# Performance work log

Hardware: AMD Instinct MI355X
Metric: run time of the kernel (lower is better)

The kernel has to match this reference:

```python
import jax, jax.numpy as jnp
import numpy as np

INF_NUMBER = 1.0e12
ZERO_TOL = 1e-9
NEG_SLOPE = 0.2

B, G, N = 16, 128, 512
P, E, K, F = 4, 1, 3, 128


def setup_inputs() -> dict:
    key = jax.random.key(0)
    k1, k2, k3, k4, k5, k6, k7 = jax.random.split(key, 7)
    x = jax.random.normal(k1, (B, G, N), dtype=jnp.float32)
    u = jax.random.uniform(k2, (B, E, N, N), dtype=jnp.float32)
    S = jnp.where(u < 0.1, u, 0.0)
    std = 1.0 / np.sqrt(G * P)
    W = jax.random.uniform(k3, (P, E, G, G), minval=-std, maxval=std, dtype=jnp.float32)
    mixer = jax.random.uniform(k4, (P, E, 2 * F), minval=-std, maxval=std, dtype=jnp.float32)
    h = jax.random.uniform(k5, (P, F, E, K, G), minval=-std, maxval=std, dtype=jnp.float32)
    b = jax.random.uniform(k6, (F, 1), minval=-std, maxval=std, dtype=jnp.float32)
    return {"x": x, "S": S, "W": W, "mixer": mixer, "h": h, "b": b}


def _attention_gso(x, W, S):
    # x: (B,G,N); W: (P,E,G,G); S: (B,E,N,N)
    # Wx = W @ x_query : (B,P,E,G,N)
    Wx = jnp.einsum('pegh,bhn->bpegn', W, x)
    # xWx = x_key @ Wx : (B,P,E,N,N)  (x_key[b,m,g] = x[b,g,m])
    xWx = jnp.einsum('bgm,bpegn->bpemn', x, Wx)
    eij = jax.nn.leaky_relu(xWx, negative_slope=NEG_SLOPE)
    # edge mask from |S| summed over edge features: (B,1,1,N,N)
    mask = (jnp.sum(jnp.abs(S), axis=1) > ZERO_TOL).astype(x.dtype)[:, None, None]
    scores = eij * mask - (1.0 - mask) * INF_NUMBER
    aij = jax.nn.softmax(scores, axis=-1) * mask
    return aij  # (B,P,E,N,N)


def reference(x, S, W, mixer, h, b):
    # mixer is declared by the torch module but unused in key-query mode
    aij = _attention_gso(x, W, S)  # (B,P,E,N,N)
    # K-hop taps: z[k] = x @ aij^k, broadcast over (P,E)
    xk = jnp.broadcast_to(x[:, None, None], (B, P, E, G, N))
    taps = [xk]
    for _ in range(1, K):
        xk = jnp.einsum('bpegn,bpenm->bpegm', xk, aij)
        taps.append(xk)
    z = jnp.stack(taps, axis=3)  # (B,P,E,K,G,N)
    # filter GEMM: contract over (E,K,G) -> (B,P,F,N)
    y = jnp.einsum('bpekgn,pfekg->bpfn', z, h) + b  # b: (F,1) broadcasts
    # concatenate heads: relu then (B, P*F, N)
    y = jax.nn.relu(y)
    y = jnp.transpose(y, (0, 3, 1, 2)).reshape(B, N, P * F)
    return jnp.transpose(y, (0, 2, 1))
```

## Files before the change

### kernel.cpp

```cpp
#include <hip/hip_runtime.h>

#define Bx 16
#define Gx 128
#define Nx 512
#define Px 4
#define Kx 3
#define Fx 128
#define NEG_SLOPE 0.2f
#define ZERO_TOL 1e-9f
#define BIGF 1.0e30f

typedef unsigned short u16;
typedef unsigned int u32;
typedef __bf16 v8bf __attribute__((ext_vector_type(8)));
typedef _Float16 v8hf __attribute__((ext_vector_type(8)));
typedef float v4f __attribute__((ext_vector_type(4)));

__device__ __forceinline__ u16 f2b(float f) {
  union { float f; u32 u; } v; v.f = f;
  u32 r = (v.u + 0x7fffu + ((v.u >> 16) & 1u)) >> 16;
  return (u16)r;
}
__device__ __forceinline__ u16 f2h(float f) {
  union { _Float16 h; u16 u; } v; v.h = (_Float16)f;
  return v.u;
}

#define G2L16(gsrc, ldst)                                                     \
  __builtin_amdgcn_global_load_lds(                                           \
      (const __attribute__((address_space(1))) void*)(gsrc),                  \
      (__attribute__((address_space(3))) void*)(ldst), 16, 0, 0)

__global__ __launch_bounds__(256) void prep_kernel(const float* __restrict__ S,
                                                   const float* __restrict__ x,
                                                   const float* __restrict__ W,
                                                   const float* __restrict__ h,
                                                   u32* __restrict__ mb,
                                                   u16* __restrict__ xb,
                                                   u16* __restrict__ xTb,
                                                   u16* __restrict__ xT16,
                                                   u16* __restrict__ w16,
                                                   u16* __restrict__ Hb) {
  const int blk = blockIdx.x;
  const int tid = threadIdx.x;
  __shared__ float t[32][33];
  if (blk < 512) {
    const int wi = blk * 256 + tid;
    const float4* S4 = (const float4*)S;
    u32 bits = 0;
#pragma unroll
    for (int q = 0; q < 8; q++) {
      float4 v = S4[(size_t)wi * 8 + q];
      bits |= (fabsf(v.x) > ZERO_TOL ? 1u : 0u) << (q * 4);
      bits |= (fabsf(v.y) > ZERO_TOL ? 2u : 0u) << (q * 4);
      bits |= (fabsf(v.z) > ZERO_TOL ? 4u : 0u) << (q * 4);
      bits |= (fabsf(v.w) > ZERO_TOL ? 8u : 0u) << (q * 4);
    }
    mb[wi] = bits;
  } else if (blk < 1536) {
    const int idx = blk - 512;
    const int b = idx >> 6, g0 = ((idx >> 4) & 3) * 32, n0 = (idx & 15) * 32;
    const int r = tid >> 3, c4 = (tid & 7) * 4;
    const float* xp = x + (size_t)b * Gx * Nx;
    float4 v = *(const float4*)&xp[(g0 + r) * Nx + n0 + c4];
    ushort4 o;
    o.x = f2b(v.x); o.y = f2b(v.y); o.z = f2b(v.z); o.w = f2b(v.w);
    *(ushort4*)&xb[(size_t)b * Gx * Nx + (g0 + r) * Nx + n0 + c4] = o;
    t[r][c4 + 0] = v.x; t[r][c4 + 1] = v.y; t[r][c4 + 2] = v.z; t[r][c4 + 3] = v.w;
    __syncthreads();
    float tv[4] = {t[c4 + 0][r], t[c4 + 1][r], t[c4 + 2][r], t[c4 + 3][r]};
    ushort4 ob, oh;
    ob.x = f2b(tv[0]); oh.x = f2h(tv[0]);
    ob.y = f2b(tv[1]); oh.y = f2h(tv[1]);
    ob.z = f2b(tv[2]); oh.z = f2h(tv[2]);
    ob.w = f2b(tv[3]); oh.w = f2h(tv[3]);
    size_t off = (size_t)b * Nx * Gx + (size_t)(n0 + r) * Gx + g0 + c4;
    *(ushort4*)&xTb[off] = ob;
    *(ushort4*)&xT16[off] = oh;
  } else if (blk < 1600) {
    int i4 = ((blk - 1536) * 256 + tid) * 4;
    float4 v = *(const float4*)&W[i4];
    ushort4 o;
    o.x = f2h(v.x); o.y = f2h(v.y); o.z = f2h(v.z); o.w = f2h(v.w);
    *(ushort4*)&w16[i4] = o;
  } else {
    int i4 = ((blk - 1600) * 256 + tid) * 4;
    float4 v = *(const float4*)&h[i4];
    ushort4 o;
    o.x = f2b(v.x); o.y = f2b(v.y); o.z = f2b(v.z); o.w = f2b(v.w);
    *(ushort4*)&Hb[i4] = o;
  }
}

__global__ __launch_bounds__(256) void wxt16_kernel(const u16* __restrict__ xT16,
                                                    const u16* __restrict__ w16,
                                                    u16* __restrict__ WxT16) {
  __shared__ __align__(16) char smem[49152];
  constexpr int OB = 16384;
  const int bp = blockIdx.x, b = bp >> 2, p = bp & 3;
  const int rt = blockIdx.y;
  const int tid = threadIdx.x;
  const int w = tid >> 6, l = tid & 63;
  const int wr = w >> 1, wc = w & 1;
  const int lr = l & 15, ks = l >> 4;

  const u16* Ap = xT16 + ((size_t)b * Nx + rt * 64) * Gx;
  const u16* Bp = w16 + (size_t)p * Gx * Gx;
#pragma unroll
  for (int it = 0; it < 4; it++) {
    int chunk = it * 256 + w * 64 + l;
    int r = chunk >> 4, kq = l & 15;
    int kg = (kq ^ (r & 15)) * 8;
    G2L16(Ap + (size_t)r * Gx + kg, smem + it * 4096 + w * 1024);
  }
#pragma unroll
  for (int it = 0; it < 8; it++) {
    int chunk = it * 256 + w * 64 + l;
    int r = chunk >> 4, kq = l & 15;
    int kg = (kq ^ (r & 15)) * 8;
    G2L16(Bp + (size_t)r * Gx + kg, smem + OB + it * 4096 + w * 1024);
  }
  __syncthreads();

  v4f acc[2][4];
#pragma unroll
  for (int fr = 0; fr < 2; fr++)
#pragma unroll
    for (int fc = 0; fc < 4; fc++) acc[fr][fc] = (v4f){0.f, 0.f, 0.f, 0.f};

#pragma unroll
  for (int t = 0; t < 4; t++) {
    int kk = t * 4 + ks;
    v8hf ah[2];
#pragma unroll
    for (int fr = 0; fr < 2; fr++) {
      int ra = wr * 32 + fr * 16 + lr;
      ah[fr] = *(const v8hf*)(smem + ra * 256 + ((kk ^ (ra & 15)) * 16));
    }
#pragma unroll
    for (int fc = 0; fc < 4; fc++) {
      int rb = wc * 64 + fc * 16 + lr;
      v8hf bh = *(const v8hf*)(smem + OB + rb * 256 + ((kk ^ (rb & 15)) * 16));
#pragma unroll
      for (int fr = 0; fr < 2; fr++)
        acc[fr][fc] = __builtin_amdgcn_mfma_f32_16x16x32_f16(ah[fr], bh, acc[fr][fc], 0, 0, 0);
    }
  }

  u16* op = WxT16 + (size_t)bp * Nx * Gx;
#pragma unroll
  for (int fr = 0; fr < 2; fr++)
#pragma unroll
    for (int fc = 0; fc < 4; fc++) {
      int n = rt * 64 + wr * 32 + fr * 16 + ks * 4;
      int g = wc * 64 + fc * 16 + lr;
#pragma unroll
      for (int q = 0; q < 4; q++) op[(size_t)(n + q) * Gx + g] = f2h(acc[fr][fc][q]);
    }
}

__global__ __launch_bounds__(512, 4) void attn5_kernel(const u16* __restrict__ xT16,
                                                       const u16* __restrict__ WxT16,
                                                       const u32* __restrict__ mb,
                                                       u16* __restrict__ aijT) {
  __shared__ __align__(16) char smem[71680];
  constexpr int OMBS = 65536, ORED = 69632;
  const int bp = blockIdx.x, b = bp >> 2;
  const int i0 = blockIdx.y * 64;
  const int tid = threadIdx.x;
  const int w = tid >> 6, l = tid & 63;
  const int wr = w >> 2, wc = w & 3;
  const int lr = l & 15, ks = l >> 4;

  {
    const u32* mbp = mb + ((size_t)b * Nx + i0) * 16;
    u32* mbs = (u32*)(smem + OMBS);
    mbs[tid] = mbp[tid];
    mbs[tid + 512] = mbp[tid + 512];
  }
  {
    const u16* Ap = xT16 + ((size_t)b * Nx + i0) * Gx;
#pragma unroll
    for (int it = 0; it < 2; it++) {
      int chunk = it * 512 + w * 64 + l;
      int r = chunk >> 4, kq = l & 15;
      int kg = (kq ^ (r & 15)) * 8;
      G2L16(Ap + (size_t)r * Gx + kg, smem + it * 8192 + w * 1024);
    }
  }
  __syncthreads();

  v8hf areg[2][4];
#pragma unroll
  for (int fr = 0; fr < 2; fr++) {
    int ra = wr * 32 + fr * 16 + lr;
#pragma unroll
    for (int t = 0; t < 4; t++) {
      int kk = t * 4 + ks;
      areg[fr][t] = *(const v8hf*)(smem + ra * 256 + ((kk ^ (ra & 15)) * 16));
    }
  }
  __syncthreads();

  const u16* Bp = WxT16 + (size_t)bp * Nx * Gx;
  auto STAGE_B = [&](int t) {
    char* dst = smem + (t & 1) * 32768;
    int g0 = t * 32;
#pragma unroll
    for (int it = 0; it < 4; it++) {
      int chunk = it * 512 + w * 64 + l;
      int r = chunk >> 2, kq = l & 3;
      int kg = (kq ^ (r & 3)) * 8;
      G2L16(Bp + (size_t)r * Gx + g0 + kg, dst + it * 8192 + w * 1024);
    }
  };

  v4f acc[2][8];
#pragma unroll
  for (int fr = 0; fr < 2; fr++)
#pragma unroll
    for (int fc = 0; fc < 8; fc++) acc[fr][fc] = (v4f){0.f, 0.f, 0.f, 0.f};

  STAGE_B(0);
  for (int t = 0; t < 4; t++) {
    __syncthreads();
    if (t < 3) STAGE_B(t + 1);
    const char* bb = smem + (t & 1) * 32768;
#pragma unroll
    for (int fc = 0; fc < 8; fc++) {
      int rb = wc * 128 + fc * 16 + lr;
      v8hf bh = *(const v8hf*)(bb + rb * 64 + ((ks ^ (rb & 3)) * 16));
#pragma unroll
      for (int fr = 0; fr < 2; fr++)
        acc[fr][fc] = __builtin_amdgcn_mfma_f32_16x16x32_f16(areg[fr][t], bh, acc[fr][fc], 0, 0, 0);
    }
  }

  u32* mbs = (u32*)(smem + OMBS);
  float* red0 = (float*)(smem + ORED);
  float* red1 = red0 + 256;

#pragma unroll
  for (int fr = 0; fr < 2; fr++)
#pragma unroll
    for (int q = 0; q < 4; q++) {
      int row = wr * 32 + fr * 16 + ks * 4 + q;
      float m = -BIGF;
#pragma unroll
      for (int fc = 0; fc < 8; fc++) {
        u32 word = mbs[row * 16 + wc * 4 + (fc >> 1)];
        int bit = ((fc & 1) << 4) + lr;
        float v = acc[fr][fc][q];
        v = v >= 0.f ? v : NEG_SLOPE * v;
        v = ((word >> bit) & 1u) ? v : -BIGF;
        acc[fr][fc][q] = v;
        m = fmaxf(m, v);
      }
      m = fmaxf(m, __shfl_xor(m, 1, 64));
      m = fmaxf(m, __shfl_xor(m, 2, 64));
      m = fmaxf(m, __shfl_xor(m, 4, 64));
      m = fmaxf(m, __shfl_xor(m, 8, 64));
      if (lr == 0) red0[row * 4 + wc] = m;
    }
  __syncthreads();
#pragma unroll
  for (int fr = 0; fr < 2; fr++)
#pragma unroll
    for (int q = 0; q < 4; q++) {
      int row = wr * 32 + fr * 16 + ks * 4 + q;
      float4 pm = *(const float4*)&red0[row * 4];
      float gm = fmaxf(fmaxf(pm.x, pm.y), fmaxf(pm.z, pm.w));
      float s = 0.f;
#pragma unroll
      for (int fc = 0; fc < 8; fc++) {
        float v = acc[fr][fc][q];
        float e = (v <= -0.5f * BIGF) ? 0.f : __expf(v - gm);
        acc[fr][fc][q] = e;
        s += e;
      }
      s += __shfl_xor(s, 1, 64);
      s += __shfl_xor(s, 2, 64);
      s += __shfl_xor(s, 4, 64);
      s += __shfl_xor(s, 8, 64);
      if (lr == 0) red1[row * 4 + wc] = s;
    }
  __syncthreads();
  u16* dst = aijT + (size_t)bp * Nx * Nx + i0;
#pragma unroll
  for (int fr = 0; fr < 2; fr++) {
    int rbase = wr * 32 + fr * 16 + ks * 4;
    float inv[4];
#pragma unroll
    for (int q = 0; q < 4; q++) {
      float4 ps = *(const float4*)&red1[(rbase + q) * 4];
      float tot = (ps.x + ps.y) + (ps.z + ps.w);
      inv[q] = tot > 0.f ? 1.f / tot : 0.f;
    }
#pragma unroll
    for (int fc = 0; fc < 8; fc++) {
      int j = wc * 128 + fc * 16 + lr;
      ushort4 pk;
      pk.x = f2b(acc[fr][fc][0] * inv[0]);
      pk.y = f2b(acc[fr][fc][1] * inv[1]);
      pk.z = f2b(acc[fr][fc][2] * inv[2]);
      pk.w = f2b(acc[fr][fc][3] * inv[3]);
      *(ushort4*)&dst[(size_t)j * Nx + rbase] = pk;
    }
  }
}

template <int MODE>
__global__ __launch_bounds__(256) void gnt_kernel(const u16* __restrict__ pA,
                                                  const u16* __restrict__ pB,
                                                  const u16* __restrict__ pC,
                                                  const u16* __restrict__ pHb,
                                                  u16* __restrict__ o1,
                                                  u16* __restrict__ o2,
                                                  float* __restrict__ oF,
                                                  const float* __restrict__ bias) {
  __shared__ __align__(16) char smem[2][12288];
  const int bp = blockIdx.x;
  const int b = bp >> 2, p = bp & 3;
  const int by = blockIdx.y;
  const int rt = (MODE == 1) ? (by >> 2) : by;
  const int ct = (MODE == 1) ? (by & 3) : 0;
  const int tid = threadIdx.x;
  const int w = tid >> 6, l = tid & 63;
  const int wr = w >> 1, wc = w & 1;
  const int lr = l & 15, kslot = l >> 4;

  constexpr int KTOT = (MODE == 2) ? (Kx * Gx) : Nx;
  constexpr int SA = (MODE == 2) ? Gx : Nx;
  constexpr int SB = (MODE == 2) ? (Kx * Gx) : Nx;
  constexpr int NT = KTOT / 32;

  const u16* Abase;
  const u16* Bbase;
  if (MODE == 0) {
    Abase = pA + (size_t)bp * Nx * Nx + (size_t)rt * 64 * Nx;
    Bbase = pB + (size_t)b * Gx * Nx;
  } else if (MODE == 1) {
    Abase = pA + (size_t)bp * Gx * Nx + (size_t)rt * 64 * Nx;
    Bbase = pB + (size_t)bp * Nx * Nx + (size_t)ct * 128 * Nx;
  } else {
    Abase = nullptr;
    Bbase = pHb + (size_t)p * Fx * (Kx * Gx);
  }

  const int sar = tid >> 2;
  const int sakg = (tid & 3) ^ (sar & 3);
  const int sbr0 = tid >> 2, sbkg0 = (tid & 3) ^ (sbr0 & 3);
  const int sbr1 = (tid + 256) >> 2, sbkg1 = (tid & 3) ^ (sbr1 & 3);

  int aoff[2], boff[4];
#pragma unroll
  for (int fr = 0; fr < 2; fr++) {
    int row = wr * 32 + fr * 16 + lr;
    aoff[fr] = row * 64 + ((kslot ^ (row & 3)) * 16);
  }
#pragma unroll
  for (int fc = 0; fc < 4; fc++) {
    int row = wc * 64 + fc * 16 + lr;
    boff[fc] = 4096 + row * 64 + ((kslot ^ (row & 3)) * 16);
  }

  auto STAGE = [&](int bufi, int k0) {
    const u16* Aseg;
    int kin;
    if (MODE == 2) {
      int seg = k0 >> 7;
      kin = k0 & 127;
      const u16* base = (seg == 0) ? (pA + (size_t)b * Nx * Gx)
                       : (seg == 1) ? (pB + (size_t)bp * Nx * Gx)
                                    : (pC + (size_t)bp * Nx * Gx);
      Aseg = base + (size_t)rt * 64 * Gx;
    } else {
      Aseg = Abase;
      kin = k0;
    }
    char* base = smem[bufi];
    G2L16(Aseg + (size_t)sar * SA + kin + sakg * 8, base + w * 1024);
    G2L16(Bbase + (size_t)sbr0 * SB + k0 + sbkg0 * 8, base + 4096 + w * 1024);
    G2L16(Bbase + (size_t)sbr1 * SB + k0 + sbkg1 * 8, base + 8192 + w * 1024);
  };

  v4f acc[2][4];
#pragma unroll
  for (int fr = 0; fr < 2; fr++)
#pragma unroll
    for (int fc = 0; fc < 4; fc++) acc[fr][fc] = (v4f){0.f, 0.f, 0.f, 0.f};

  STAGE(0, 0);
  int cur = 0;
  for (int t = 0; t < NT; t++) {
    __syncthreads();
    if (t + 1 < NT) STAGE(cur ^ 1, (t + 1) * 32);
    const char* bb = smem[cur];
    v8bf af[2], bf4[4];
#pragma unroll
    for (int fr = 0; fr < 2; fr++) af[fr] = *(const v8bf*)(bb + aoff[fr]);
#pragma unroll
    for (int fc = 0; fc < 4; fc++) bf4[fc] = *(const v8bf*)(bb + boff[fc]);
#pragma unroll
    for (int fr = 0; fr < 2; fr++)
#pragma unroll
      for (int fc = 0; fc < 4; fc++)
        acc[fr][fc] = __builtin_amdgcn_mfma_f32_16x16x32_bf16(af[fr], bf4[fc],
                                                              acc[fr][fc], 0, 0, 0);
    cur ^= 1;
  }

  if (MODE == 0) {
    u16* z1p = o1 + (size_t)bp * Gx * Nx;
    u16* z1Tp = o2 + (size_t)bp * Nx * Gx;
#pragma unroll
    for (int fr = 0; fr < 2; fr++)
#pragma unroll
      for (int fc = 0; fc < 4; fc++) {
        int m0 = rt * 64 + wr * 32 + fr * 16 + kslot * 4;
        int g = wc * 64 + fc * 16 + lr;
        v4f a = acc[fr][fc];
        ushort4 pk;
        pk.x = f2b(a[0]); pk.y = f2b(a[1]); pk.z = f2b(a[2]); pk.w = f2b(a[3]);
        *(ushort4*)&z1p[(size_t)g * Nx + m0] = pk;
        z1Tp[(size_t)(m0 + 0) * Gx + g] = pk.x;
        z1Tp[(size_t)(m0 + 1) * Gx + g] = pk.y;
        z1Tp[(size_t)(m0 + 2) * Gx + g] = pk.z;
        z1Tp[(size_t)(m0 + 3) * Gx + g] = pk.w;
      }
  } else if (MODE == 1) {
    u16* z2Tp = o1 + (size_t)bp * Nx * Gx;
#pragma unroll
    for (int fr = 0; fr < 2; fr++)
#pragma unroll
      for (int fc = 0; fc < 4; fc++) {
        int g0r = rt * 64 + wr * 32 + fr * 16 + kslot * 4;
        int m = ct * 128 + wc * 64 + fc * 16 + lr;
        v4f a = acc[fr][fc];
        ushort4 pk;
        pk.x = f2b(a[0]); pk.y = f2b(a[1]); pk.z = f2b(a[2]); pk.w = f2b(a[3]);
        *(ushort4*)&z2Tp[(size_t)m * Gx + g0r] = pk;
      }
  } else {
    float* op = oF + (size_t)(b * Px + p) * Fx * Nx;
#pragma unroll
    for (int fc = 0; fc < 4; fc++) {
      int f = wc * 64 + fc * 16 + lr;
      float bi = bias[f];
#pragma unroll
      for (int fr = 0; fr < 2; fr++) {
        int n0 = rt * 64 + wr * 32 + fr * 16 + kslot * 4;
        v4f a = acc[fr][fc];
        float4 o;
        o.x = fmaxf(a[0] + bi, 0.f);
        o.y = fmaxf(a[1] + bi, 0.f);
        o.z = fmaxf(a[2] + bi, 0.f);
        o.w = fmaxf(a[3] + bi, 0.f);
        *(float4*)&op[(size_t)f * Nx + n0] = o;
      }
    }
  }
}

extern "C" void kernel_launch(void* const* d_in, const int* in_sizes, int n_in,
                              void* d_out, int out_size, void* d_ws, size_t ws_size,
                              hipStream_t stream) {
  const float* x = (const float*)d_in[0];
  const float* S = (const float*)d_in[1];
  const float* W = (const float*)d_in[2];
  const float* h = (const float*)d_in[4];
  const float* bias = (const float*)d_in[5];
  float* out = (float*)d_out;

  char* ws = (char*)d_ws;
  u16* aijT  = (u16*)ws;
  u16* WxT16 = (u16*)(ws + 33554432);
  u16* xT16  = (u16*)(ws + 41943040);
  u16* xTb   = (u16*)(ws + 44040192);
  u16* xb    = (u16*)(ws + 46137344);
  u16* z1    = (u16*)(ws + 48234496);
  u16* z1T   = (u16*)(ws + 56623104);
  u16* z2T   = (u16*)(ws + 65011712);
  u16* Hb    = (u16*)(ws + 73400320);
  u16* W16   = (u16*)(ws + 73793536);
  u32* mb    = (u32*)(ws + 73924608);

  prep_kernel<<<dim3(1792), 256, 0, stream>>>(S, x, W, h, mb, xb, xTb, xT16, W16, Hb);
  wxt16_kernel<<<dim3(Bx * Px, Nx / 64), 256, 0, stream>>>(xT16, W16, WxT16);
  attn5_kernel<<<dim3(Bx * Px, Nx / 64), 512, 0, stream>>>(xT16, WxT16, mb, aijT);
  gnt_kernel<0><<<dim3(Bx * Px, 8), 256, 0, stream>>>(aijT, xb, nullptr, nullptr,
                                                      z1, z1T, nullptr, nullptr);
  gnt_kernel<1><<<dim3(Bx * Px, 8), 256, 0, stream>>>(z1, aijT, nullptr, nullptr,
                                                      z2T, nullptr, nullptr, nullptr);
  gnt_kernel<2><<<dim3(Bx * Px, 8), 256, 0, stream>>>(xTb, z1T, z2T, Hb,
                                                      nullptr, nullptr, out, bias);
  (void)in_sizes; (void)n_in; (void)out_size; (void)ws_size;
}
```

Measured before the change: 78.82 us.

## Fuse second hop with filter GEMM and single-buffer attention staging

Fuses the second K-hop GEMM with the filter GEMM, so z2 stays in LDS as a swizzled tile instead of being written to global memory and read back. This removes one launch and the z2T round trip. The attention kernel drops double buffering of the Wx tiles to shrink LDS from about 70KB to 38KB, trading copy/compute overlap for more resident blocks. The mask-packing prep now uses wave ballots over coalesced loads instead of per-thread float4 bit packing.

```diff
diff --git a/kernel.cpp b/kernel.cpp
--- a/kernel.cpp
+++ b/kernel.cpp
@@ -12,6 +12,7 @@
 
 typedef unsigned short u16;
 typedef unsigned int u32;
+typedef unsigned long long u64;
 typedef __bf16 v8bf __attribute__((ext_vector_type(8)));
 typedef _Float16 v8hf __attribute__((ext_vector_type(8)));
 typedef float v4f __attribute__((ext_vector_type(4)));
@@ -45,18 +46,14 @@
   const int tid = threadIdx.x;
   __shared__ float t[32][33];
   if (blk < 512) {
-    const int wi = blk * 256 + tid;
-    const float4* S4 = (const float4*)S;
-    u32 bits = 0;
-#pragma unroll
-    for (int q = 0; q < 8; q++) {
-      float4 v = S4[(size_t)wi * 8 + q];
-      bits |= (fabsf(v.x) > ZERO_TOL ? 1u : 0u) << (q * 4);
-      bits |= (fabsf(v.y) > ZERO_TOL ? 2u : 0u) << (q * 4);
-      bits |= (fabsf(v.z) > ZERO_TOL ? 4u : 0u) << (q * 4);
-      bits |= (fabsf(v.w) > ZERO_TOL ? 8u : 0u) << (q * 4);
-    }
-    mb[wi] = bits;
+    const int w = tid >> 6, l = tid & 63;
+    const size_t base = (size_t)blk * 8192;
+#pragma unroll 4
+    for (int i = 0; i < 32; i++) {
+      float v = S[base + i * 256 + tid];
+      u64 m = __ballot(fabsf(v) > ZERO_TOL);
+      if (l == 0) *(u64*)&mb[(base + i * 256 + w * 64) >> 5] = m;
+    }
   } else if (blk < 1536) {
     const int idx = blk - 512;
     const int b = idx >> 6, g0 = ((idx >> 4) & 3) * 32, n0 = (idx & 15) * 32;
@@ -159,12 +156,12 @@
     }
 }
 
-__global__ __launch_bounds__(512, 4) void attn5_kernel(const u16* __restrict__ xT16,
+__global__ __launch_bounds__(512, 4) void attn7_kernel(const u16* __restrict__ xT16,
                                                        const u16* __restrict__ WxT16,
                                                        const u32* __restrict__ mb,
                                                        u16* __restrict__ aijT) {
-  __shared__ __align__(16) char smem[71680];
-  constexpr int OMBS = 65536, ORED = 69632;
+  __shared__ __align__(16) char smem[38912];
+  constexpr int OMBS = 32768, ORED = 36864;
   const int bp = blockIdx.x, b = bp >> 2;
   const int i0 = blockIdx.y * 64;
   const int tid = threadIdx.x;
@@ -202,38 +199,32 @@
   }
   __syncthreads();
 
+  v4f acc[2][8];
+#pragma unroll
+  for (int fr = 0; fr < 2; fr++)
+#pragma unroll
+    for (int fc = 0; fc < 8; fc++) acc[fr][fc] = (v4f){0.f, 0.f, 0.f, 0.f};
+
   const u16* Bp = WxT16 + (size_t)bp * Nx * Gx;
-  auto STAGE_B = [&](int t) {
-    char* dst = smem + (t & 1) * 32768;
+  for (int t = 0; t < 4; t++) {
     int g0 = t * 32;
 #pragma unroll
     for (int it = 0; it < 4; it++) {
       int chunk = it * 512 + w * 64 + l;
       int r = chunk >> 2, kq = l & 3;
       int kg = (kq ^ (r & 3)) * 8;
-      G2L16(Bp + (size_t)r * Gx + g0 + kg, dst + it * 8192 + w * 1024);
-    }
-  };
-
-  v4f acc[2][8];
-#pragma unroll
-  for (int fr = 0; fr < 2; fr++)
-#pragma unroll
-    for (int fc = 0; fc < 8; fc++) acc[fr][fc] = (v4f){0.f, 0.f, 0.f, 0.f};
-
-  STAGE_B(0);
-  for (int t = 0; t < 4; t++) {
+      G2L16(Bp + (size_t)r * Gx + g0 + kg, smem + it * 8192 + w * 1024);
+    }
     __syncthreads();
-    if (t < 3) STAGE_B(t + 1);
-    const char* bb = smem + (t & 1) * 32768;
 #pragma unroll
     for (int fc = 0; fc < 8; fc++) {
       int rb = wc * 128 + fc * 16 + lr;
-      v8hf bh = *(const v8hf*)(bb + rb * 64 + ((ks ^ (rb & 3)) * 16));
+      v8hf bh = *(const v8hf*)(smem + rb * 64 + ((ks ^ (rb & 3)) * 16));
 #pragma unroll
       for (int fr = 0; fr < 2; fr++)
         acc[fr][fc] = __builtin_amdgcn_mfma_f32_16x16x32_f16(areg[fr][t], bh, acc[fr][fc], 0, 0, 0);
     }
+    __syncthreads();
   }
 
   u32* mbs = (u32*)(smem + OMBS);
@@ -309,43 +300,21 @@
   }
 }
 
-template <int MODE>
-__global__ __launch_bounds__(256) void gnt_kernel(const u16* __restrict__ pA,
-                                                  const u16* __restrict__ pB,
-                                                  const u16* __restrict__ pC,
-                                                  const u16* __restrict__ pHb,
-                                                  u16* __restrict__ o1,
-                                                  u16* __restrict__ o2,
-                                                  float* __restrict__ oF,
-                                                  const float* __restrict__ bias) {
+__global__ __launch_bounds__(256) void hop1_kernel(const u16* __restrict__ pA,
+                                                   const u16* __restrict__ pB,
+                                                   u16* __restrict__ o1,
+                                                   u16* __restrict__ o2) {
   __shared__ __align__(16) char smem[2][12288];
   const int bp = blockIdx.x;
-  const int b = bp >> 2, p = bp & 3;
-  const int by = blockIdx.y;
-  const int rt = (MODE == 1) ? (by >> 2) : by;
-  const int ct = (MODE == 1) ? (by & 3) : 0;
+  const int b = bp >> 2;
+  const int rt = blockIdx.y;
   const int tid = threadIdx.x;
   const int w = tid >> 6, l = tid & 63;
   const int wr = w >> 1, wc = w & 1;
   const int lr = l & 15, kslot = l >> 4;
 
-  constexpr int KTOT = (MODE == 2) ? (Kx * Gx) : Nx;
-  constexpr int SA = (MODE == 2) ? Gx : Nx;
-  constexpr int SB = (MODE == 2) ? (Kx * Gx) : Nx;
-  constexpr int NT = KTOT / 32;
-
-  const u16* Abase;
-  const u16* Bbase;
-  if (MODE == 0) {
-    Abase = pA + (size_t)bp * Nx * Nx + (size_t)rt * 64 * Nx;
-    Bbase = pB + (size_t)b * Gx * Nx;
-  } else if (MODE == 1) {
-    Abase = pA + (size_t)bp * Gx * Nx + (size_t)rt * 64 * Nx;
-    Bbase = pB + (size_t)bp * Nx * Nx + (size_t)ct * 128 * Nx;
-  } else {
-    Abase = nullptr;
-    Bbase = pHb + (size_t)p * Fx * (Kx * Gx);
-  }
+  const u16* Abase = pA + (size_t)bp * Nx * Nx + (size_t)rt * 64 * Nx;
+  const u16* Bbase = pB + (size_t)b * Gx * Nx;
 
   const int sar = tid >> 2;
   const int sakg = (tid & 3) ^ (sar & 3);
@@ -365,23 +334,10 @@
   }
 
   auto STAGE = [&](int bufi, int k0) {
-    const u16* Aseg;
-    int kin;
-    if (MODE == 2) {
-      int seg = k0 >> 7;
-      kin = k0 & 127;
-      const u16* base = (seg == 0) ? (pA + (size_t)b * Nx * Gx)
-                       : (seg == 1) ? (pB + (size_t)bp * Nx * Gx)
-                                    : (pC + (size_t)bp * Nx * Gx);
-      Aseg = base + (size_t)rt * 64 * Gx;
-    } else {
-      Aseg = Abase;
-      kin = k0;
-    }
     char* base = smem[bufi];
-    G2L16(Aseg + (size_t)sar * SA + kin + sakg * 8, base + w * 1024);
-    G2L16(Bbase + (size_t)sbr0 * SB + k0 + sbkg0 * 8, base + 4096 + w * 1024);
-    G2L16(Bbase + (size_t)sbr1 * SB + k0 + sbkg1 * 8, base + 8192 + w * 1024);
+    G2L16(Abase + (size_t)sar * Nx + k0 + sakg * 8, base + w * 1024);
+    G2L16(Bbase + (size_t)sbr0 * Nx + k0 + sbkg0 * 8, base + 4096 + w * 1024);
+    G2L16(Bbase + (size_t)sbr1 * Nx + k0 + sbkg1 * 8, base + 8192 + w * 1024);
   };
 
   v4f acc[2][4];
@@ -392,9 +348,9 @@
 
   STAGE(0, 0);
   int cur = 0;
-  for (int t = 0; t < NT; t++) {
+  for (int t = 0; t < 16; t++) {
     __syncthreads();
-    if (t + 1 < NT) STAGE(cur ^ 1, (t + 1) * 32);
+    if (t + 1 < 16) STAGE(cur ^ 1, (t + 1) * 32);
     const char* bb = smem[cur];
     v8bf af[2], bf4[4];
 #pragma unroll
@@ -410,54 +366,177 @@
     cur ^= 1;
   }
 
-  if (MODE == 0) {
-    u16* z1p = o1 + (size_t)bp * Gx * Nx;
-    u16* z1Tp = o2 + (size_t)bp * Nx * Gx;
+  u16* z1p = o1 + (size_t)bp * Gx * Nx;
+  u16* z1Tp = o2 + (size_t)bp * Nx * Gx;
+#pragma unroll
+  for (int fr = 0; fr < 2; fr++)
+#pragma unroll
+    for (int fc = 0; fc < 4; fc++) {
+      int m0 = rt * 64 + wr * 32 + fr * 16 + kslot * 4;
+      int g = wc * 64 + fc * 16 + lr;
+      v4f a = acc[fr][fc];
+      ushort4 pk;
+      pk.x = f2b(a[0]); pk.y = f2b(a[1]); pk.z = f2b(a[2]); pk.w = f2b(a[3]);
+      *(ushort4*)&z1p[(size_t)g * Nx + m0] = pk;
+      z1Tp[(size_t)(m0 + 0) * Gx + g] = pk.x;
+      z1Tp[(size_t)(m0 + 1) * Gx + g] = pk.y;
+      z1Tp[(size_t)(m0 + 2) * Gx + g] = pk.z;
+      z1Tp[(size_t)(m0 + 3) * Gx + g] = pk.w;
+    }
+}
+
+__global__ __launch_bounds__(256) void hop2filt_kernel(const u16* __restrict__ aijT,
+                                                       const u16* __restrict__ z1,
+                                                       const u16* __restrict__ z1T,
+                                                       const u16* __restrict__ xTb,
+                                                       const u16* __restrict__ Hb,
+                                                       const float* __restrict__ bias,
+                                                       float* __restrict__ out) {
+  __shared__ __align__(16) char smem[2 * 12288 + 16384];
+  constexpr int OT = 24576;
+  const int bp = blockIdx.x, b = bp >> 2, p = bp & 3;
+  const int rt = blockIdx.y;
+  const int tid = threadIdx.x;
+  const int w = tid >> 6, l = tid & 63;
+  const int wr = w >> 1, wc = w & 1;
+  const int lr = l & 15, kslot = l >> 4;
+
+  const int sar = tid >> 2;
+  const int sakg = (tid & 3) ^ (sar & 3);
+  const int sbr0 = tid >> 2, sbkg0 = (tid & 3) ^ (sbr0 & 3);
+  const int sbr1 = (tid + 256) >> 2, sbkg1 = (tid & 3) ^ (sbr1 & 3);
+
+  int aoff[2], boff[4];
+#pragma unroll
+  for (int fr = 0; fr < 2; fr++) {
+    int row = wr * 32 + fr * 16 + lr;
+    aoff[fr] = row * 64 + ((kslot ^ (row & 3)) * 16);
+  }
+#pragma unroll
+  for (int fc = 0; fc < 4; fc++) {
+    int row = wc * 64 + fc * 16 + lr;
+    boff[fc] = 4096 + row * 64 + ((kslot ^ (row & 3)) * 16);
+  }
+
+  const u16* A1 = aijT + (size_t)bp * Nx * Nx + (size_t)rt * 64 * Nx;
+  const u16* B1 = z1 + (size_t)bp * Gx * Nx;
+  auto STAGE1 = [&](int bufi, int k0) {
+    char* base = smem + bufi * 12288;
+    G2L16(A1 + (size_t)sar * Nx + k0 + sakg * 8, base + w * 1024);
+    G2L16(B1 + (size_t)sbr0 * Nx + k0 + sbkg0 * 8, base + 4096 + w * 1024);
+    G2L16(B1 + (size_t)sbr1 * Nx + k0 + sbkg1 * 8, base + 8192 + w * 1024);
+  };
+
+  v4f acc[2][4];
+#pragma unroll
+  for (int fr = 0; fr < 2; fr++)
+#pragma unroll
+    for (int fc = 0; fc < 4; fc++) acc[fr][fc] = (v4f){0.f, 0.f, 0.f, 0.f};
+
+  STAGE1(0, 0);
+  int cur = 0;
+  for (int t = 0; t < 16; t++) {
+    __syncthreads();
+    if (t + 1 < 16) STAGE1(cur ^ 1, (t + 1) * 32);
+    const char* bb = smem + cur * 12288;
+    v8bf af[2], bf4[4];
+#pragma unroll
+    for (int fr = 0; fr < 2; fr++) af[fr] = *(const v8bf*)(bb + aoff[fr]);
+#pragma unroll
+    for (int fc = 0; fc < 4; fc++) bf4[fc] = *(const v8bf*)(bb + boff[fc]);
 #pragma unroll
     for (int fr = 0; fr < 2; fr++)
 #pragma unroll
+      for (int fc = 0; fc < 4; fc++)
+        acc[fr][fc] = __builtin_amdgcn_mfma_f32_16x16x32_bf16(af[fr], bf4[fc],
+                                                              acc[fr][fc], 0, 0, 0);
+    cur ^= 1;
+  }
+
+  {
+    char* T = smem + OT;
+#pragma unroll
+    for (int fr = 0; fr < 2; fr++)
+#pragma unroll
       for (int fc = 0; fc < 4; fc++) {
-        int m0 = rt * 64 + wr * 32 + fr * 16 + kslot * 4;
+        int m0 = wr * 32 + fr * 16 + kslot * 4;
         int g = wc * 64 + fc * 16 + lr;
         v4f a = acc[fr][fc];
-        ushort4 pk;
-        pk.x = f2b(a[0]); pk.y = f2b(a[1]); pk.z = f2b(a[2]); pk.w = f2b(a[3]);
-        *(ushort4*)&z1p[(size_t)g * Nx + m0] = pk;
-        z1Tp[(size_t)(m0 + 0) * Gx + g] = pk.x;
-        z1Tp[(size_t)(m0 + 1) * Gx + g] = pk.y;
-        z1Tp[(size_t)(m0 + 2) * Gx + g] = pk.z;
-        z1Tp[(size_t)(m0 + 3) * Gx + g] = pk.w;
+#pragma unroll
+        for (int q = 0; q < 4; q++) {
+          int row = m0 + q;
+          *(u16*)(T + row * 256 + ((g * 2) ^ ((row & 7) << 4))) = f2b(a[q]);
+        }
       }
-  } else if (MODE == 1) {
-    u16* z2Tp = o1 + (size_t)bp * Nx * Gx;
+  }
+  __syncthreads();
+
+  const u16* A2s0 = xTb + (size_t)b * Nx * Gx + (size_t)rt * 64 * Gx;
+  const u16* A2s1 = z1T + (size_t)bp * Nx * Gx + (size_t)rt * 64 * Gx;
+  const u16* B2 = Hb + (size_t)p * Fx * (Kx * Gx);
+  auto STAGE2 = [&](int bufi, int k0) {
+    char* base = smem + bufi * 12288;
+    if (k0 < 256) {
+      const u16* Aseg = (k0 < 128) ? A2s0 : A2s1;
+      int kin = k0 & 127;
+      G2L16(Aseg + (size_t)sar * Gx + kin + sakg * 8, base + w * 1024);
+    }
+    G2L16(B2 + (size_t)sbr0 * (Kx * Gx) + k0 + sbkg0 * 8, base + 4096 + w * 1024);
+    G2L16(B2 + (size_t)sbr1 * (Kx * Gx) + k0 + sbkg1 * 8, base + 8192 + w * 1024);
+  };
+
+  v4f acc2[2][4];
+#pragma unroll
+  for (int fr = 0; fr < 2; fr++)
+#pragma unroll
+    for (int fc = 0; fc < 4; fc++) acc2[fr][fc] = (v4f){0.f, 0.f, 0.f, 0.f};
+
+  STAGE2(0, 0);
+  cur = 0;
+  for (int t = 0; t < 12; t++) {
+    __syncthreads();
+    if (t + 1 < 12) STAGE2(cur ^ 1, (t + 1) * 32);
+    const char* bb = smem + cur * 12288;
+    v8bf af[2], bf4[4];
+    if (t < 8) {
+#pragma unroll
+      for (int fr = 0; fr < 2; fr++) af[fr] = *(const v8bf*)(bb + aoff[fr]);
+    } else {
+      const char* T = smem + OT;
+      int tl = t - 8;
+#pragma unroll
+      for (int fr = 0; fr < 2; fr++) {
+        int row = wr * 32 + fr * 16 + lr;
+        af[fr] = *(const v8bf*)(T + row * 256 +
+                                ((tl * 64 + kslot * 16) ^ ((row & 7) << 4)));
+      }
+    }
+#pragma unroll
+    for (int fc = 0; fc < 4; fc++) bf4[fc] = *(const v8bf*)(bb + boff[fc]);
 #pragma unroll
     for (int fr = 0; fr < 2; fr++)
 #pragma unroll
-      for (int fc = 0; fc < 4; fc++) {
-        int g0r = rt * 64 + wr * 32 + fr * 16 + kslot * 4;
-        int m = ct * 128 + wc * 64 + fc * 16 + lr;
-        v4f a = acc[fr][fc];
-        ushort4 pk;
-        pk.x = f2b(a[0]); pk.y = f2b(a[1]); pk.z = f2b(a[2]); pk.w = f2b(a[3]);
-        *(ushort4*)&z2Tp[(size_t)m * Gx + g0r] = pk;
-      }
-  } else {
-    float* op = oF + (size_t)(b * Px + p) * Fx * Nx;
-#pragma unroll
-    for (int fc = 0; fc < 4; fc++) {
-      int f = wc * 64 + fc * 16 + lr;
-      float bi = bias[f];
-#pragma unroll
-      for (int fr = 0; fr < 2; fr++) {
-        int n0 = rt * 64 + wr * 32 + fr * 16 + kslot * 4;
-        v4f a = acc[fr][fc];
-        float4 o;
-        o.x = fmaxf(a[0] + bi, 0.f);
-        o.y = fmaxf(a[1] + bi, 0.f);
-        o.z = fmaxf(a[2] + bi, 0.f);
-        o.w = fmaxf(a[3] + bi, 0.f);
-        *(float4*)&op[(size_t)f * Nx + n0] = o;
-      }
+      for (int fc = 0; fc < 4; fc++)
+        acc2[fr][fc] = __builtin_amdgcn_mfma_f32_16x16x32_bf16(af[fr], bf4[fc],
+                                                               acc2[fr][fc], 0, 0, 0);
+    cur ^= 1;
+  }
+
+  float* op = out + (size_t)(b * Px + p) * Fx * Nx;
+#pragma unroll
+  for (int fc = 0; fc < 4; fc++) {
+    int f = wc * 64 + fc * 16 + lr;
+    float bi = bias[f];
+#pragma unroll
+    for (int fr = 0; fr < 2; fr++) {
+      int n0 = rt * 64 + wr * 32 + fr * 16 + kslot * 4;
+      v4f a = acc2[fr][fc];
+      float4 o;
+      o.x = fmaxf(a[0] + bi, 0.f);
+      o.y = fmaxf(a[1] + bi, 0.f);
+      o.z = fmaxf(a[2] + bi, 0.f);
+      o.w = fmaxf(a[3] + bi, 0.f);
+      *(float4*)&op[(size_t)f * Nx + n0] = o;
     }
   }
 }
@@ -480,19 +559,14 @@
   u16* xb    = (u16*)(ws + 46137344);
   u16* z1    = (u16*)(ws + 48234496);
   u16* z1T   = (u16*)(ws + 56623104);
-  u16* z2T   = (u16*)(ws + 65011712);
   u16* Hb    = (u16*)(ws + 73400320);
   u16* W16   = (u16*)(ws + 73793536);
   u32* mb    = (u32*)(ws + 73924608);
 
   prep_kernel<<<dim3(1792), 256, 0, stream>>>(S, x, W, h, mb, xb, xTb, xT16, W16, Hb);
   wxt16_kernel<<<dim3(Bx * Px, Nx / 64), 256, 0, stream>>>(xT16, W16, WxT16);
-  attn5_kernel<<<dim3(Bx * Px, Nx / 64), 512, 0, stream>>>(xT16, WxT16, mb, aijT);
-  gnt_kernel<0><<<dim3(Bx * Px, 8), 256, 0, stream>>>(aijT, xb, nullptr, nullptr,
-                                                      z1, z1T, nullptr, nullptr);
-  gnt_kernel<1><<<dim3(Bx * Px, 8), 256, 0, stream>>>(z1, aijT, nullptr, nullptr,
-                                                      z2T, nullptr, nullptr, nullptr);
-  gnt_kernel<2><<<dim3(Bx * Px, 8), 256, 0, stream>>>(xTb, z1T, z2T, Hb,
-                                                      nullptr, nullptr, out, bias);
+  attn7_kernel<<<dim3(Bx * Px, Nx / 64), 512, 0, stream>>>(xT16, WxT16, mb, aijT);
+  hop1_kernel<<<dim3(Bx * Px, 8), 256, 0, stream>>>(aijT, xb, z1, z1T);
+  hop2filt_kernel<<<dim3(Bx * Px, 8), 256, 0, stream>>>(aijT, z1, z1T, xTb, Hb, bias, out);
   (void)in_sizes; (void)n_in; (void)out_size; (void)ws_size;
 }
```

Result: no change. 77.83 us (-1.3%).
